# Performance work log

Hardware: AMD Instinct MI355X
Metric: run time of the kernel (lower is better)

The kernel has to match this reference:

```python
import jax, jax.numpy as jnp
import numpy as np

N = 20000
E = 640000
F_IN = 128
HID = 64
HEADS = 4
OUT = 10
NUM_GRAPHS = 128
NEG_SLOPE = 0.2
BN_EPS = 1e-5


def setup_inputs() -> dict:
    key = jax.random.key(0)
    ks = jax.random.split(key, 24)
    x = jax.random.normal(ks[0], (N, F_IN), dtype=jnp.float32)
    edge_index = jax.random.randint(ks[1], (2, E), 0, N, dtype=jnp.int32)
    batch = jnp.sort(jax.random.randint(ks[2], (N,), 0, NUM_GRAPHS, dtype=jnp.int32))
    s = 0.05
    HC = HEADS * HID  # 256
    inp = {
        'x': x, 'edge_index': edge_index, 'batch': batch,
        # GATConv 1: in=128 -> heads*64, concat
        'W1': jax.random.normal(ks[3], (F_IN, HC)) * s,
        'as1': jax.random.normal(ks[4], (HEADS, HID)) * s,
        'ad1': jax.random.normal(ks[5], (HEADS, HID)) * s,
        'b1': jnp.zeros((HC,), jnp.float32),
        'g1': jnp.ones((HC,), jnp.float32),
        'be1': jnp.zeros((HC,), jnp.float32),
        # GATConv 2: in=256 -> heads*64, concat
        'W2': jax.random.normal(ks[6], (HC, HC)) * s,
        'as2': jax.random.normal(ks[7], (HEADS, HID)) * s,
        'ad2': jax.random.normal(ks[8], (HEADS, HID)) * s,
        'b2': jnp.zeros((HC,), jnp.float32),
        'g2': jnp.ones((HC,), jnp.float32),
        'be2': jnp.zeros((HC,), jnp.float32),
        # GATConv 3: in=256 -> 64, concat=False (mean over heads)
        'W3': jax.random.normal(ks[9], (HC, HC)) * s,
        'as3': jax.random.normal(ks[10], (HEADS, HID)) * s,
        'ad3': jax.random.normal(ks[11], (HEADS, HID)) * s,
        'b3': jnp.zeros((HID,), jnp.float32),
        # final Linear 64 -> 10
        'Wlin': jax.random.normal(ks[12], (HID, OUT)) * s,
        'blin': jnp.zeros((OUT,), jnp.float32),
    }
    return inp


def _gat_conv(x, src, dst, W, a_src, a_dst, b, concat):
    # PyG GATConv: h = x @ W -> [N,H,C]; alpha_e = leaky_relu(as[src]+ad[dst]);
    # softmax over edges grouped by destination; scatter-add alpha*h[src].
    h = (x @ W).reshape(N, HEADS, HID)
    a_s = jnp.einsum('nhc,hc->nh', h, a_src)  # [N,H]
    a_d = jnp.einsum('nhc,hc->nh', h, a_dst)
    e = jax.nn.leaky_relu(a_s[src] + a_d[dst], NEG_SLOPE)  # [E,H]
    m = jax.ops.segment_max(e, dst, num_segments=N)  # per-dst max, stable softmax
    e = jnp.exp(e - m[dst])
    denom = jax.ops.segment_sum(e, dst, num_segments=N)
    alpha = e / (denom[dst] + 1e-16)  # [E,H]
    out = jax.ops.segment_sum(h[src] * alpha[:, :, None], dst, num_segments=N)  # [N,H,C]
    if concat:
        out = out.reshape(N, HEADS * HID)
    else:
        out = out.mean(axis=1)
    return out + b


def _bn(x, g, b):
    # BatchNorm1d (training-mode batch statistics)
    mu = x.mean(0)
    var = x.var(0)
    return (x - mu) * jax.lax.rsqrt(var + BN_EPS) * g + b


def reference(x, edge_index, batch, W1, as1, ad1, b1, g1, be1,
              W2, as2, ad2, b2, g2, be2, W3, as3, ad3, b3, Wlin, blin):
    # add self-loops (PyG GATConv default add_self_loops=True)
    loops = jnp.arange(N, dtype=edge_index.dtype)
    src = jnp.concatenate([edge_index[0], loops])
    dst = jnp.concatenate([edge_index[1], loops])

    xs = []
    h = _gat_conv(x, src, dst, W1, as1, ad1, b1, concat=True)
    h = _bn(h, g1, be1)
    xs.append(h)
    h = jax.nn.elu(h)  # dropout is identity in eval mode

    h = _gat_conv(h, src, dst, W2, as2, ad2, b2, concat=True)
    h = _bn(h, g2, be2)
    xs.append(h)
    h = jax.nn.elu(h)

    h = _gat_conv(h, src, dst, W3, as3, ad3, b3, concat=False)
    xs.append(h)

    # global_mean_pool over graphs
    sums = jax.ops.segment_sum(h, batch, num_segments=NUM_GRAPHS)
    cnt = jax.ops.segment_sum(jnp.ones((N,), h.dtype), batch, num_segments=NUM_GRAPHS)
    pooled = sums / jnp.maximum(cnt, 1.0)[:, None]
    xs.append(pooled)

    out = pooled @ Wlin + blin
    return (out, *xs)
```

## Files before the change

kernel.cpp:

```cpp
#include <hip/hip_runtime.h>
#include <hip/hip_bf16.h>
#include <math.h>

#define N_NODES 20000
#define N_EDGES 640000
#define F_IN 128
#define HID 64
#define HEADS 4
#define HC 256
#define OUT_DIM 10
#define NUM_GRAPHS 128
#define NEG_SLOPE 0.2f
#define BN_EPS 1e-5f
#define CONV_N (N_NODES * F_IN / 4)
#define ELL_CAP 128

typedef short bf16s;
using bf16x8 = __attribute__((ext_vector_type(8))) short;
using bf16x4 = __attribute__((ext_vector_type(4))) short;
using f32x4 = __attribute__((ext_vector_type(4))) float;

__device__ __forceinline__ float bs2f(short s) {
    unsigned int u = ((unsigned int)(unsigned short)s) << 16;
    return __builtin_bit_cast(float, u);
}
__device__ __forceinline__ short f2bs(float f) {
    unsigned int u = __builtin_bit_cast(unsigned int, f);
    unsigned int r = u + 0x7FFFu + ((u >> 16) & 1u);
    return (short)(r >> 16);
}


__global__ void prep_all(const float* __restrict__ x, bf16s* __restrict__ xb,
                         const float* __restrict__ W1, const float* __restrict__ W2,
                         const float* __restrict__ W3,
                         bf16s* __restrict__ Wt1, bf16s* __restrict__ Wt2,
                         bf16s* __restrict__ Wt3,
                         int* __restrict__ cnt, int* __restrict__ ell,
                         float* __restrict__ colstats, int* __restrict__ counter) {
    int tid = blockIdx.x * blockDim.x + threadIdx.x;
    if (tid < CONV_N) {
        float4 v = reinterpret_cast<const float4*>(x)[tid];
        bf16x4 o;
        o[0] = f2bs(v.x); o[1] = f2bs(v.y); o[2] = f2bs(v.z); o[3] = f2bs(v.w);
        reinterpret_cast<bf16x4*>(xb)[tid] = o;
        return;
    }
    tid -= CONV_N;
    if (tid < HC * F_IN) { int c = tid >> 7, k = tid & 127; Wt1[tid] = f2bs(W1[(size_t)k * HC + c]); return; }
    tid -= HC * F_IN;
    if (tid < HC * HC) { int c = tid >> 8, k = tid & 255; Wt2[tid] = f2bs(W2[(size_t)k * HC + c]); return; }
    tid -= HC * HC;
    if (tid < HC * HC) { int c = tid >> 8, k = tid & 255; Wt3[tid] = f2bs(W3[(size_t)k * HC + c]); return; }
    tid -= HC * HC;
    if (tid < N_NODES) {
        cnt[tid] = 1;
        ell[(size_t)tid * ELL_CAP] = tid;
        return;
    }
    tid -= N_NODES;
    if (tid < 2 * HC) { colstats[tid] = 0.f; return; }
    tid -= 2 * HC;
    if (tid == 0) *counter = 0;
}


__global__ void fill_ell(const int* __restrict__ ei, int* cnt, int* __restrict__ ell, int E) {
    int tid = blockIdx.x * blockDim.x + threadIdx.x;
    if (tid < E) {
        int src = ei[tid];
        int dst = ei[E + tid];
        int pos = atomicAdd(&cnt[dst], 1);
        if (pos < ELL_CAP) ell[(size_t)dst * ELL_CAP + pos] = src;
    }
}


__global__ __launch_bounds__(256) void gemm_bf16(
        const bf16s* __restrict__ A, const bf16s* __restrict__ Wt,
        bf16s* __restrict__ Hout,
        const float* __restrict__ a_src, const float* __restrict__ a_dst,
        float* __restrict__ asb, float* __restrict__ adb,
        int M, int K) {
    __shared__ bf16s As[128][72];
    __shared__ bf16s Bs[64][72];
    int tid = threadIdx.x;
    int wave = tid >> 6, lane = tid & 63;
    int row0 = blockIdx.x * 128;
    int head = blockIdx.y;
    int col0 = head * 64;
    int lr = lane & 15, lk = lane >> 4;

    f32x4 acc[2][4];
    #pragma unroll
    for (int i = 0; i < 2; i++)
        #pragma unroll
        for (int j = 0; j < 4; j++)
            acc[i][j] = (f32x4){0.f, 0.f, 0.f, 0.f};

    for (int k0 = 0; k0 < K; k0 += 64) {
        #pragma unroll
        for (int i = 0; i < 4; i++) {
            int idx = tid + i * 256;
            int r = idx >> 3, ch = idx & 7;
            int gr = row0 + r;
            bf16x8 v = {};
            if (gr < M) v = *reinterpret_cast<const bf16x8*>(A + (size_t)gr * K + k0 + ch * 8);
            *reinterpret_cast<bf16x8*>(&As[r][ch * 8]) = v;
        }
        #pragma unroll
        for (int i = 0; i < 2; i++) {
            int idx = tid + i * 256;
            int r = idx >> 3, ch = idx & 7;
            bf16x8 v = *reinterpret_cast<const bf16x8*>(Wt + (size_t)(col0 + r) * K + k0 + ch * 8);
            *reinterpret_cast<bf16x8*>(&Bs[r][ch * 8]) = v;
        }
        __syncthreads();
        #pragma unroll
        for (int ks = 0; ks < 2; ks++) {
            bf16x8 bfr[4];
            #pragma unroll
            for (int j = 0; j < 4; j++)
                bfr[j] = *reinterpret_cast<const bf16x8*>(&Bs[j * 16 + lr][ks * 32 + lk * 8]);
            #pragma unroll
            for (int i = 0; i < 2; i++) {
                bf16x8 afr = *reinterpret_cast<const bf16x8*>(&As[wave * 32 + i * 16 + lr][ks * 32 + lk * 8]);
                #pragma unroll
                for (int j = 0; j < 4; j++)
                    acc[i][j] = __builtin_amdgcn_mfma_f32_16x16x32_bf16(afr, bfr[j], acc[i][j], 0, 0, 0);
            }
        }
        __syncthreads();
    }

    #pragma unroll
    for (int i = 0; i < 2; i++) {
        #pragma unroll
        for (int q = 0; q < 4; q++) {
            int r = row0 + wave * 32 + i * 16 + lk * 4 + q;
            if (r < M) {
                #pragma unroll
                for (int j = 0; j < 4; j++) {
                    int c = col0 + j * 16 + lr;
                    Hout[(size_t)r * HC + c] = f2bs(acc[i][j][q]);
                }
            }
        }
    }

    float asv0 = a_src[col0 + 0 * 16 + lr], asv1 = a_src[col0 + 1 * 16 + lr];
    float asv2 = a_src[col0 + 2 * 16 + lr], asv3 = a_src[col0 + 3 * 16 + lr];
    float adv0 = a_dst[col0 + 0 * 16 + lr], adv1 = a_dst[col0 + 1 * 16 + lr];
    float adv2 = a_dst[col0 + 2 * 16 + lr], adv3 = a_dst[col0 + 3 * 16 + lr];
    #pragma unroll
    for (int i = 0; i < 2; i++) {
        #pragma unroll
        for (int q = 0; q < 4; q++) {
            float ps = acc[i][0][q] * asv0 + acc[i][1][q] * asv1 + acc[i][2][q] * asv2 + acc[i][3][q] * asv3;
            float pd = acc[i][0][q] * adv0 + acc[i][1][q] * adv1 + acc[i][2][q] * adv2 + acc[i][3][q] * adv3;
            #pragma unroll
            for (int off = 1; off < 16; off <<= 1) {
                ps += __shfl_xor(ps, off);
                pd += __shfl_xor(pd, off);
            }
            int r = row0 + wave * 32 + i * 16 + lk * 4 + q;
            if (lr == 0 && r < M) {
                asb[r * HEADS + head] = ps;
                adb[r * HEADS + head] = pd;
            }
        }
    }
}


__device__ __forceinline__ float lrelu(float x) { return x > 0.f ? x : NEG_SLOPE * x; }

template<int MODE>
__global__ __launch_bounds__(256) void gat_aggregate(
        const bf16s* __restrict__ hfeat,
        const float* __restrict__ asb, const float* __restrict__ adb,
        const int* __restrict__ cnt, const int* __restrict__ ell,
        const float* __restrict__ bias,
        float* __restrict__ out) {
    __shared__ float4 exps[4][ELL_CAP];
    __shared__ int    srcs[4][ELL_CAP];
    int wid = threadIdx.x >> 6, lane = threadIdx.x & 63;
    int d = blockIdx.x * 4 + wid;
    int deg = min(cnt[d], ELL_CAP);
    const int* row = ell + (size_t)d * ELL_CAP;

    float adv0 = adb[d * HEADS + 0], adv1 = adb[d * HEADS + 1];
    float adv2 = adb[d * HEADS + 2], adv3 = adb[d * HEADS + 3];

    float s0 = 0.f, s1 = 0.f, s2 = 0.f, s3 = 0.f;
    for (int j = lane; j < deg; j += 64) {
        int s = row[j];
        const float4 av = *reinterpret_cast<const float4*>(asb + (size_t)s * HEADS);
        float e0 = __expf(lrelu(av.x + adv0));
        float e1 = __expf(lrelu(av.y + adv1));
        float e2 = __expf(lrelu(av.z + adv2));
        float e3 = __expf(lrelu(av.w + adv3));
        float4 ev; ev.x = e0; ev.y = e1; ev.z = e2; ev.w = e3;
        exps[wid][j] = ev;
        srcs[wid][j] = s;
        s0 += e0; s1 += e1; s2 += e2; s3 += e3;
    }
    #pragma unroll
    for (int off = 32; off > 0; off >>= 1) {
        s0 += __shfl_xor(s0, off);
        s1 += __shfl_xor(s1, off);
        s2 += __shfl_xor(s2, off);
        s3 += __shfl_xor(s3, off);
    }
    float r0 = 1.f / (s0 + 1e-16f), r1 = 1.f / (s1 + 1e-16f);
    float r2 = 1.f / (s2 + 1e-16f), r3 = 1.f / (s3 + 1e-16f);

    int half = lane >> 5;
    int cl = lane & 31;
    int hsel = cl >> 3;
    float rdh = (hsel == 0) ? r0 : (hsel == 1) ? r1 : (hsel == 2) ? r2 : r3;
    const float* expf_base = reinterpret_cast<const float*>(&exps[wid][0]);

    float a0 = 0.f, a1 = 0.f, a2 = 0.f, a3 = 0.f, a4 = 0.f, a5 = 0.f, a6 = 0.f, a7 = 0.f;
    float b0 = 0.f, b1 = 0.f, b2 = 0.f, b3 = 0.f, b4 = 0.f, b5 = 0.f, b6 = 0.f, b7 = 0.f;

    int nfull = deg & ~3;
    for (int j = 0; j < nfull; j += 4) {
        int iA = j + half;
        int iB = j + 2 + half;
        int sA = srcs[wid][iA];
        int sB = srcs[wid][iB];
        float alA = expf_base[iA * 4 + hsel] * rdh;
        float alB = expf_base[iB * 4 + hsel] * rdh;
        const bf16x8 vA = *reinterpret_cast<const bf16x8*>(hfeat + (size_t)sA * HC + cl * 8);
        const bf16x8 vB = *reinterpret_cast<const bf16x8*>(hfeat + (size_t)sB * HC + cl * 8);
        a0 += alA * bs2f(vA[0]); a1 += alA * bs2f(vA[1]);
        a2 += alA * bs2f(vA[2]); a3 += alA * bs2f(vA[3]);
        a4 += alA * bs2f(vA[4]); a5 += alA * bs2f(vA[5]);
        a6 += alA * bs2f(vA[6]); a7 += alA * bs2f(vA[7]);
        b0 += alB * bs2f(vB[0]); b1 += alB * bs2f(vB[1]);
        b2 += alB * bs2f(vB[2]); b3 += alB * bs2f(vB[3]);
        b4 += alB * bs2f(vB[4]); b5 += alB * bs2f(vB[5]);
        b6 += alB * bs2f(vB[6]); b7 += alB * bs2f(vB[7]);
    }
    for (int j = nfull + half; j < deg; j += 2) {
        int s = srcs[wid][j];
        float al = expf_base[j * 4 + hsel] * rdh;
        const bf16x8 v = *reinterpret_cast<const bf16x8*>(hfeat + (size_t)s * HC + cl * 8);
        a0 += al * bs2f(v[0]); a1 += al * bs2f(v[1]);
        a2 += al * bs2f(v[2]); a3 += al * bs2f(v[3]);
        a4 += al * bs2f(v[4]); a5 += al * bs2f(v[5]);
        a6 += al * bs2f(v[6]); a7 += al * bs2f(v[7]);
    }
    float av0 = a0 + b0, av1 = a1 + b1, av2 = a2 + b2, av3 = a3 + b3;
    float av4 = a4 + b4, av5 = a5 + b5, av6 = a6 + b6, av7 = a7 + b7;

    av0 += __shfl_xor(av0, 32); av1 += __shfl_xor(av1, 32);
    av2 += __shfl_xor(av2, 32); av3 += __shfl_xor(av3, 32);
    av4 += __shfl_xor(av4, 32); av5 += __shfl_xor(av5, 32);
    av6 += __shfl_xor(av6, 32); av7 += __shfl_xor(av7, 32);

    if constexpr (MODE == 0) {
        if (half == 0) {
            const float4 bb0 = *reinterpret_cast<const float4*>(bias + cl * 8);
            const float4 bb1 = *reinterpret_cast<const float4*>(bias + cl * 8 + 4);
            av0 += bb0.x; av1 += bb0.y; av2 += bb0.z; av3 += bb0.w;
            av4 += bb1.x; av5 += bb1.y; av6 += bb1.z; av7 += bb1.w;
            float4 o0; o0.x = av0; o0.y = av1; o0.z = av2; o0.w = av3;
            float4 o1; o1.x = av4; o1.y = av5; o1.z = av6; o1.w = av7;
            *reinterpret_cast<float4*>(out + (size_t)d * HC + cl * 8) = o0;
            *reinterpret_cast<float4*>(out + (size_t)d * HC + cl * 8 + 4) = o1;
        }
    } else {
        float h0 = av0 + __shfl_xor(av0, 8); h0 += __shfl_xor(h0, 16);
        float h1 = av1 + __shfl_xor(av1, 8); h1 += __shfl_xor(h1, 16);
        float h2 = av2 + __shfl_xor(av2, 8); h2 += __shfl_xor(h2, 16);
        float h3 = av3 + __shfl_xor(av3, 8); h3 += __shfl_xor(h3, 16);
        float h4 = av4 + __shfl_xor(av4, 8); h4 += __shfl_xor(h4, 16);
        float h5 = av5 + __shfl_xor(av5, 8); h5 += __shfl_xor(h5, 16);
        float h6 = av6 + __shfl_xor(av6, 8); h6 += __shfl_xor(h6, 16);
        float h7 = av7 + __shfl_xor(av7, 8); h7 += __shfl_xor(h7, 16);
        if (half == 0 && cl < 8) {
            int c = cl * 8;
            float4 o0, o1;
            o0.x = 0.25f * h0 + bias[c + 0]; o0.y = 0.25f * h1 + bias[c + 1];
            o0.z = 0.25f * h2 + bias[c + 2]; o0.w = 0.25f * h3 + bias[c + 3];
            o1.x = 0.25f * h4 + bias[c + 4]; o1.y = 0.25f * h5 + bias[c + 5];
            o1.z = 0.25f * h6 + bias[c + 6]; o1.w = 0.25f * h7 + bias[c + 7];
            *reinterpret_cast<float4*>(out + (size_t)d * HID + c) = o0;
            *reinterpret_cast<float4*>(out + (size_t)d * HID + c + 4) = o1;
        }
    }
}


__global__ void bn_stats_fin(const float* __restrict__ x, float* colsum, float* colsq,
                             const float* __restrict__ g, const float* __restrict__ be,
                             float* scale, float* shift, int* counter, int n) {
    __shared__ int lastFlag;
    int col = threadIdx.x;
    float s = 0.f, q = 0.f;
    for (int r = blockIdx.x; r < n; r += gridDim.x) {
        float v = x[(size_t)r * HC + col];
        s += v;
        q += v * v;
    }
    atomicAdd(&colsum[col], s);
    atomicAdd(&colsq[col], q);
    __syncthreads();
    if (threadIdx.x == 0) {
        __threadfence();
        int prev = atomicAdd(counter, 1);
        lastFlag = (prev == (int)gridDim.x - 1) ? 1 : 0;
    }
    __syncthreads();
    if (lastFlag) {
        __threadfence();
        float cs = ((volatile float*)colsum)[col];
        float cq = ((volatile float*)colsq)[col];
        float mu = cs / (float)n;
        float var = cq / (float)n - mu * mu;
        float sc = g[col] * rsqrtf(var + BN_EPS);
        scale[col] = sc;
        shift[col] = be[col] - mu * sc;
        colsum[col] = 0.f;
        colsq[col] = 0.f;
        if (threadIdx.x == 0) *counter = 0;
    }
}

__global__ void bn_apply_elu(const float* __restrict__ x,
                             const float* __restrict__ scale, const float* __restrict__ shift,
                             float* __restrict__ xs_out, bf16s* __restrict__ act, int n) {
    int col = threadIdx.x;
    float sc = scale[col], sh = shift[col];
    for (int r = blockIdx.x; r < n; r += gridDim.x) {
        float v = x[(size_t)r * HC + col];
        float y = v * sc + sh;
        xs_out[(size_t)r * HC + col] = y;
        float e = y > 0.f ? y : __expf(y) - 1.f;
        act[(size_t)r * HC + col] = f2bs(e);
    }
}


__global__ __launch_bounds__(256) void pool_final(
        const float* __restrict__ xs2, const int* __restrict__ batch,
        const float* __restrict__ Wlin, const float* __restrict__ blin,
        float* __restrict__ pooled_out, float* __restrict__ out_final) {
    __shared__ float red[4][HID];
    int g = blockIdx.x;
    int tid = threadIdx.x;
    int w = tid >> 6, lane = tid & 63;

    int lo = 0, hi = N_NODES;
    while (lo < hi) { int mid = (lo + hi) >> 1; if (batch[mid] < g) lo = mid + 1; else hi = mid; }
    int a = lo;
    lo = 0; hi = N_NODES;
    while (lo < hi) { int mid = (lo + hi) >> 1; if (batch[mid] < g + 1) lo = mid + 1; else hi = mid; }
    int b = lo;

    float acc = 0.f;
    for (int n = a + w; n < b; n += 4) acc += xs2[(size_t)n * HID + lane];
    red[w][lane] = acc;
    __syncthreads();

    if (w == 0) {
        float pooled = (red[0][lane] + red[1][lane] + red[2][lane] + red[3][lane])
                       / fmaxf((float)(b - a), 1.f);
        pooled_out[g * HID + lane] = pooled;
        #pragma unroll
        for (int o = 0; o < OUT_DIM; o++) {
            float p = pooled * Wlin[lane * OUT_DIM + o];
            #pragma unroll
            for (int off = 32; off > 0; off >>= 1) p += __shfl_xor(p, off);
            if (lane == 0) out_final[g * OUT_DIM + o] = p + blin[o];
        }
    }
}


extern "C" void kernel_launch(void* const* d_in, const int* in_sizes, int n_in,
                              void* d_out, int out_size, void* d_ws, size_t ws_size,
                              hipStream_t stream) {
    const float* x     = (const float*)d_in[0];
    const int*   ei    = (const int*)d_in[1];
    const int*   batch = (const int*)d_in[2];
    const float* W1  = (const float*)d_in[3];
    const float* as1 = (const float*)d_in[4];
    const float* ad1 = (const float*)d_in[5];
    const float* b1  = (const float*)d_in[6];
    const float* g1  = (const float*)d_in[7];
    const float* be1 = (const float*)d_in[8];
    const float* W2  = (const float*)d_in[9];
    const float* as2 = (const float*)d_in[10];
    const float* ad2 = (const float*)d_in[11];
    const float* b2  = (const float*)d_in[12];
    const float* g2  = (const float*)d_in[13];
    const float* be2 = (const float*)d_in[14];
    const float* W3  = (const float*)d_in[15];
    const float* as3 = (const float*)d_in[16];
    const float* ad3 = (const float*)d_in[17];
    const float* b3  = (const float*)d_in[18];
    const float* Wlin = (const float*)d_in[19];
    const float* blin = (const float*)d_in[20];

    float* out_final = (float*)d_out;
    float* xs0 = out_final + NUM_GRAPHS * OUT_DIM;
    float* xs1 = xs0 + (size_t)N_NODES * HC;
    float* xs2 = xs1 + (size_t)N_NODES * HC;
    float* pooled_out = xs2 + (size_t)N_NODES * HID;

    char* p = (char*)d_ws;
    auto alloc = [&](size_t bytes) { char* r = p; p += (bytes + 255) & ~(size_t)255; return (void*)r; };
    bf16s* hfeat  = (bf16s*)alloc((size_t)N_NODES * HC * 2);
    bf16s* actC   = (bf16s*)alloc((size_t)N_NODES * HC * 2);
    bf16s* xb     = (bf16s*)alloc((size_t)N_NODES * F_IN * 2);
    float* gatB   = (float*)alloc((size_t)N_NODES * HC * 4);
    bf16s* Wt1    = (bf16s*)alloc((size_t)HC * F_IN * 2);
    bf16s* Wt2    = (bf16s*)alloc((size_t)HC * HC * 2);
    bf16s* Wt3    = (bf16s*)alloc((size_t)HC * HC * 2);
    float* asb    = (float*)alloc((size_t)N_NODES * HEADS * 4);
    float* adb    = (float*)alloc((size_t)N_NODES * HEADS * 4);
    int*   cnt    = (int*)alloc((size_t)N_NODES * 4);
    int*   ell    = (int*)alloc((size_t)N_NODES * ELL_CAP * 4);
    float* colstats = (float*)alloc(2 * HC * 4);
    float* colsum = colstats;
    float* colsq  = colstats + HC;
    float* scale  = (float*)alloc(HC * 4);
    float* shift  = (float*)alloc(HC * 4);
    int*   counter = (int*)alloc(256);

    const int PREP_TOT = CONV_N + HC * F_IN + 2 * HC * HC + N_NODES + 2 * HC + 1;

    prep_all<<<(PREP_TOT + 255) / 256, 256, 0, stream>>>(x, xb, W1, W2, W3, Wt1, Wt2, Wt3,
                                                         cnt, ell, colstats, counter);
    fill_ell<<<(N_EDGES + 255) / 256, 256, 0, stream>>>(ei, cnt, ell, N_EDGES);

    int agg_blocks = N_NODES / 4;
    dim3 ggrid((N_NODES + 127) / 128, HEADS);

    {
        gemm_bf16<<<ggrid, 256, 0, stream>>>(xb, Wt1, hfeat, as1, ad1, asb, adb, N_NODES, F_IN);
        gat_aggregate<0><<<agg_blocks, 256, 0, stream>>>(hfeat, asb, adb, cnt, ell, b1, gatB);
        bn_stats_fin<<<512, 256, 0, stream>>>(gatB, colsum, colsq, g1, be1, scale, shift, counter, N_NODES);
        bn_apply_elu<<<2048, 256, 0, stream>>>(gatB, scale, shift, xs0, actC, N_NODES);
    }
    {
        gemm_bf16<<<ggrid, 256, 0, stream>>>(actC, Wt2, hfeat, as2, ad2, asb, adb, N_NODES, HC);
        gat_aggregate<0><<<agg_blocks, 256, 0, stream>>>(hfeat, asb, adb, cnt, ell, b2, gatB);
        bn_stats_fin<<<512, 256, 0, stream>>>(gatB, colsum, colsq, g2, be2, scale, shift, counter, N_NODES);
        bn_apply_elu<<<2048, 256, 0, stream>>>(gatB, scale, shift, xs1, actC, N_NODES);
    }
    {
        gemm_bf16<<<ggrid, 256, 0, stream>>>(actC, Wt3, hfeat, as3, ad3, asb, adb, N_NODES, HC);
        gat_aggregate<1><<<agg_blocks, 256, 0, stream>>>(hfeat, asb, adb, cnt, ell, b3, xs2);
    }
    pool_final<<<NUM_GRAPHS, 256, 0, stream>>>(xs2, batch, Wlin, blin, pooled_out, out_final);
}
```

Baseline: 296.0 us.

## Widen GEMM tile to two heads per block and store ELL indices as u16

The GEMM block now computes 128 output columns (two heads) instead of 64, so each A tile is loaded once for twice the MFMA work, and the grid's head dimension is halved. Separately, ELL neighbour indices are stored as 16-bit unsigned shorts, halving the index footprint and bandwidth in fill_ell and the aggregation. The wider tile raises accumulator register pressure and shared memory use, which can lower occupancy. N=20000 fits in 16 bits, but the ELL format now relies on node ids staying below 65536.

```diff
diff --git a/kernel.cpp b/kernel.cpp
--- a/kernel.cpp
+++ b/kernel.cpp
@@ -16,6 +16,7 @@
 #define ELL_CAP 128
 
 typedef short bf16s;
+typedef unsigned short u16;
 using bf16x8 = __attribute__((ext_vector_type(8))) short;
 using bf16x4 = __attribute__((ext_vector_type(4))) short;
 using f32x4 = __attribute__((ext_vector_type(4))) float;
@@ -36,7 +37,7 @@
                          const float* __restrict__ W3,
                          bf16s* __restrict__ Wt1, bf16s* __restrict__ Wt2,
                          bf16s* __restrict__ Wt3,
-                         int* __restrict__ cnt, int* __restrict__ ell,
+                         int* __restrict__ cnt, u16* __restrict__ ell,
                          float* __restrict__ colstats, int* __restrict__ counter) {
     int tid = blockIdx.x * blockDim.x + threadIdx.x;
     if (tid < CONV_N) {
@@ -55,7 +56,7 @@
     tid -= HC * HC;
     if (tid < N_NODES) {
         cnt[tid] = 1;
-        ell[(size_t)tid * ELL_CAP] = tid;
+        ell[(size_t)tid * ELL_CAP] = (u16)tid;
         return;
     }
     tid -= N_NODES;
@@ -65,13 +66,13 @@
 }
 
 
-__global__ void fill_ell(const int* __restrict__ ei, int* cnt, int* __restrict__ ell, int E) {
+__global__ void fill_ell(const int* __restrict__ ei, int* cnt, u16* __restrict__ ell, int E) {
     int tid = blockIdx.x * blockDim.x + threadIdx.x;
     if (tid < E) {
         int src = ei[tid];
         int dst = ei[E + tid];
         int pos = atomicAdd(&cnt[dst], 1);
-        if (pos < ELL_CAP) ell[(size_t)dst * ELL_CAP + pos] = src;
+        if (pos < ELL_CAP) ell[(size_t)dst * ELL_CAP + pos] = (u16)src;
     }
 }
 
@@ -83,19 +84,19 @@
         float* __restrict__ asb, float* __restrict__ adb,
         int M, int K) {
     __shared__ bf16s As[128][72];
-    __shared__ bf16s Bs[64][72];
+    __shared__ bf16s Bs[128][72];
     int tid = threadIdx.x;
     int wave = tid >> 6, lane = tid & 63;
     int row0 = blockIdx.x * 128;
-    int head = blockIdx.y;
-    int col0 = head * 64;
+    int head2 = blockIdx.y;
+    int col0 = head2 * 128;
     int lr = lane & 15, lk = lane >> 4;
 
-    f32x4 acc[2][4];
+    f32x4 acc[2][8];
     #pragma unroll
     for (int i = 0; i < 2; i++)
         #pragma unroll
-        for (int j = 0; j < 4; j++)
+        for (int j = 0; j < 8; j++)
             acc[i][j] = (f32x4){0.f, 0.f, 0.f, 0.f};
 
     for (int k0 = 0; k0 < K; k0 += 64) {
@@ -109,7 +110,7 @@
             *reinterpret_cast<bf16x8*>(&As[r][ch * 8]) = v;
         }
         #pragma unroll
-        for (int i = 0; i < 2; i++) {
+        for (int i = 0; i < 4; i++) {
             int idx = tid + i * 256;
             int r = idx >> 3, ch = idx & 7;
             bf16x8 v = *reinterpret_cast<const bf16x8*>(Wt + (size_t)(col0 + r) * K + k0 + ch * 8);
@@ -118,15 +119,15 @@
         __syncthreads();
         #pragma unroll
         for (int ks = 0; ks < 2; ks++) {
-            bf16x8 bfr[4];
+            bf16x8 bfr[8];
             #pragma unroll
-            for (int j = 0; j < 4; j++)
+            for (int j = 0; j < 8; j++)
                 bfr[j] = *reinterpret_cast<const bf16x8*>(&Bs[j * 16 + lr][ks * 32 + lk * 8]);
             #pragma unroll
             for (int i = 0; i < 2; i++) {
                 bf16x8 afr = *reinterpret_cast<const bf16x8*>(&As[wave * 32 + i * 16 + lr][ks * 32 + lk * 8]);
                 #pragma unroll
-                for (int j = 0; j < 4; j++)
+                for (int j = 0; j < 8; j++)
                     acc[i][j] = __builtin_amdgcn_mfma_f32_16x16x32_bf16(afr, bfr[j], acc[i][j], 0, 0, 0);
             }
         }
@@ -140,7 +141,7 @@
             int r = row0 + wave * 32 + i * 16 + lk * 4 + q;
             if (r < M) {
                 #pragma unroll
-                for (int j = 0; j < 4; j++) {
+                for (int j = 0; j < 8; j++) {
                     int c = col0 + j * 16 + lr;
                     Hout[(size_t)r * HC + c] = f2bs(acc[i][j][q]);
                 }
@@ -148,25 +149,33 @@
         }
     }
 
-    float asv0 = a_src[col0 + 0 * 16 + lr], asv1 = a_src[col0 + 1 * 16 + lr];
-    float asv2 = a_src[col0 + 2 * 16 + lr], asv3 = a_src[col0 + 3 * 16 + lr];
-    float adv0 = a_dst[col0 + 0 * 16 + lr], adv1 = a_dst[col0 + 1 * 16 + lr];
-    float adv2 = a_dst[col0 + 2 * 16 + lr], adv3 = a_dst[col0 + 3 * 16 + lr];
+    float asv[8], adv[8];
+    #pragma unroll
+    for (int j = 0; j < 8; j++) {
+        asv[j] = a_src[col0 + j * 16 + lr];
+        adv[j] = a_dst[col0 + j * 16 + lr];
+    }
     #pragma unroll
     for (int i = 0; i < 2; i++) {
         #pragma unroll
         for (int q = 0; q < 4; q++) {
-            float ps = acc[i][0][q] * asv0 + acc[i][1][q] * asv1 + acc[i][2][q] * asv2 + acc[i][3][q] * asv3;
-            float pd = acc[i][0][q] * adv0 + acc[i][1][q] * adv1 + acc[i][2][q] * adv2 + acc[i][3][q] * adv3;
+            float ps0 = acc[i][0][q] * asv[0] + acc[i][1][q] * asv[1] + acc[i][2][q] * asv[2] + acc[i][3][q] * asv[3];
+            float pd0 = acc[i][0][q] * adv[0] + acc[i][1][q] * adv[1] + acc[i][2][q] * adv[2] + acc[i][3][q] * adv[3];
+            float ps1 = acc[i][4][q] * asv[4] + acc[i][5][q] * asv[5] + acc[i][6][q] * asv[6] + acc[i][7][q] * asv[7];
+            float pd1 = acc[i][4][q] * adv[4] + acc[i][5][q] * adv[5] + acc[i][6][q] * adv[6] + acc[i][7][q] * adv[7];
             #pragma unroll
             for (int off = 1; off < 16; off <<= 1) {
-                ps += __shfl_xor(ps, off);
-                pd += __shfl_xor(pd, off);
+                ps0 += __shfl_xor(ps0, off);
+                pd0 += __shfl_xor(pd0, off);
+                ps1 += __shfl_xor(ps1, off);
+                pd1 += __shfl_xor(pd1, off);
             }
             int r = row0 + wave * 32 + i * 16 + lk * 4 + q;
             if (lr == 0 && r < M) {
-                asb[r * HEADS + head] = ps;
-                adb[r * HEADS + head] = pd;
+                asb[r * HEADS + head2 * 2 + 0] = ps0;
+                adb[r * HEADS + head2 * 2 + 0] = pd0;
+                asb[r * HEADS + head2 * 2 + 1] = ps1;
+                adb[r * HEADS + head2 * 2 + 1] = pd1;
             }
         }
     }
@@ -179,7 +188,7 @@
 __global__ __launch_bounds__(256) void gat_aggregate(
         const bf16s* __restrict__ hfeat,
         const float* __restrict__ asb, const float* __restrict__ adb,
-        const int* __restrict__ cnt, const int* __restrict__ ell,
+        const int* __restrict__ cnt, const u16* __restrict__ ell,
         const float* __restrict__ bias,
         float* __restrict__ out) {
     __shared__ float4 exps[4][ELL_CAP];
@@ -187,7 +196,7 @@
     int wid = threadIdx.x >> 6, lane = threadIdx.x & 63;
     int d = blockIdx.x * 4 + wid;
     int deg = min(cnt[d], ELL_CAP);
-    const int* row = ell + (size_t)d * ELL_CAP;
+    const u16* row = ell + (size_t)d * ELL_CAP;
 
     float adv0 = adb[d * HEADS + 0], adv1 = adb[d * HEADS + 1];
     float adv2 = adb[d * HEADS + 2], adv3 = adb[d * HEADS + 3];
@@ -423,7 +432,7 @@
     float* asb    = (float*)alloc((size_t)N_NODES * HEADS * 4);
     float* adb    = (float*)alloc((size_t)N_NODES * HEADS * 4);
     int*   cnt    = (int*)alloc((size_t)N_NODES * 4);
-    int*   ell    = (int*)alloc((size_t)N_NODES * ELL_CAP * 4);
+    u16*   ell    = (u16*)alloc((size_t)N_NODES * ELL_CAP * 2);
     float* colstats = (float*)alloc(2 * HC * 4);
     float* colsum = colstats;
     float* colsq  = colstats + HC;
@@ -438,7 +447,7 @@
     fill_ell<<<(N_EDGES + 255) / 256, 256, 0, stream>>>(ei, cnt, ell, N_EDGES);
 
     int agg_blocks = N_NODES / 4;
-    dim3 ggrid((N_NODES + 127) / 128, HEADS);
+    dim3 ggrid((N_NODES + 127) / 128, HEADS / 2);
 
     {
         gemm_bf16<<<ggrid, 256, 0, stream>>>(xb, Wt1, hfeat, as1, ad1, asb, adb, N_NODES, F_IN);
```

Result: no change. 296.0 us (+0.0%).
